# Performance work log

Hardware: AMD Instinct MI355X
Metric: run time of the kernel (lower is better)

The kernel has to match this reference:

```python
import jax, jax.numpy as jnp
import numpy as np

T, P, E, H = 200000, 100000, 600000, 256

def setup_inputs() -> dict:
    key = jax.random.key(0)
    ks = jax.random.split(key, 8)
    x = jax.random.normal(ks[0], (T, H), dtype=jnp.float32)
    points = jax.random.normal(ks[1], (P, 3), dtype=jnp.float32)
    triangles = jax.random.randint(ks[2], (T, 3), 0, P)
    triangle_edges = jax.random.randint(ks[3], (2, E), 0, T)
    din = H + 9
    W1 = jax.random.normal(ks[4], (din, H), dtype=jnp.float32) / np.sqrt(din)
    b1 = jnp.zeros((H,), dtype=jnp.float32)
    W2 = jax.random.normal(ks[5], (H, H), dtype=jnp.float32) / np.sqrt(H)
    b2 = jnp.zeros((H,), dtype=jnp.float32)
    return {"x": x, "points": points, "triangles": triangles,
            "triangle_edges": triangle_edges, "W1": W1, "b1": b1, "W2": W2, "b2": b2}

def reference(x, points, triangles, triangle_edges, W1, b1, W2, b2):
    # Per-triangle geometry: [T, 3(corners), 3(xyz)]
    tp = points[triangles]
    e_ij = tp[:, 0] - tp[:, 1]
    e_ik = tp[:, 0] - tp[:, 2]
    e_jk = tp[:, 1] - tp[:, 2]
    edge_vectors = jnp.stack([e_ij, e_ik, e_jk], axis=1)  # [T,3,3]
    t_max = jnp.max(edge_vectors, axis=1).astype(x.dtype)  # [T,3]
    t_min = jnp.min(edge_vectors, axis=1).astype(x.dtype)  # [T,3]
    barycenters = jnp.mean(tp, axis=1).astype(x.dtype)     # [T,3]

    src = triangle_edges[0]
    tgt = triangle_edges[1]
    # Relative geometric descriptor per edge: [E, 9]
    r_n_k = jnp.concatenate([t_min[src] - t_min[tgt],
                             t_max[src] - t_max[tgt],
                             barycenters[src] - barycenters[tgt]], axis=1)
    feature_diff = x[src] - x[tgt]                          # [E, H]
    mlp_in = jnp.concatenate([r_n_k, feature_diff], axis=1)  # [E, H+9]
    h = jax.nn.relu(mlp_in @ W1 + b1)
    mlp_out = h @ W2 + b2                                   # [E, H]
    # Scatter-add back to source triangles (order-independent sum)
    new_features = jax.ops.segment_sum(mlp_out, src, num_segments=x.shape[0])
    return new_features.astype(x.dtype)
```

## Files before the change

### kernel.cpp

```cpp
#include <hip/hip_runtime.h>
#include <stdint.h>

typedef float f32x4v __attribute__((ext_vector_type(4)));
typedef short short8v __attribute__((ext_vector_type(8)));

__device__ __forceinline__ float bf2f(unsigned short u) {
  union { uint32_t i; float f; } v; v.i = ((uint32_t)u) << 16; return v.f;
}
__device__ __forceinline__ unsigned short f2bf(float f) {
  union { float f; uint32_t i; } v; v.f = f;
  uint32_t x = v.i;
  uint32_t r = (x + 0x7FFFu + ((x >> 16) & 1u)) >> 16;
  return (unsigned short)r;
}

__global__ void zero_kernel(int* __restrict__ p, int n4) {
  int i = blockIdx.x * blockDim.x + threadIdx.x;
  int stride = gridDim.x * blockDim.x;
  for (; i < n4; i += stride) ((int4*)p)[i] = make_int4(0, 0, 0, 0);
}

__global__ void setup_kernel(const float* __restrict__ W1, const float* __restrict__ W2,
                             const float* __restrict__ points, const int* __restrict__ tri,
                             const int* __restrict__ te,
                             unsigned short* __restrict__ W1fT, unsigned short* __restrict__ W2T,
                             float* __restrict__ geo12, int* __restrict__ count,
                             int T, int E) {
  int i = blockIdx.x * blockDim.x + threadIdx.x;
  if (i < 256 * 288) {
    int n = i / 288, k = i % 288;
    float v = 0.f;
    if (k < 256) v = W1[(9 + k) * 256 + n];
    else if (k < 265) v = W1[(k - 256) * 256 + n];
    W1fT[i] = f2bf(v);
  }
  if (i < 256 * 256) {
    int n = i >> 8, k = i & 255;
    W2T[i] = f2bf(W2[k * 256 + n]);
  }
  if (i < T) {
    int t = i;
    int i0 = tri[3 * t], i1 = tri[3 * t + 1], i2 = tri[3 * t + 2];
    float g[12];
#pragma unroll
    for (int c = 0; c < 3; ++c) {
      float p0 = points[i0 * 3 + c], p1 = points[i1 * 3 + c], p2 = points[i2 * 3 + c];
      float e0 = p0 - p1, e1 = p0 - p2, e2 = p1 - p2;
      float mx = fmaxf(e0, fmaxf(e1, e2));
      float mn = fminf(e0, fminf(e1, e2));
      float bc = (p0 + p1 + p2) * (1.0f / 3.0f);
      g[c] = mn; g[3 + c] = mx; g[6 + c] = bc;
    }
    g[9] = 0.f; g[10] = 0.f; g[11] = 0.f;
    float4* o = (float4*)(geo12 + (size_t)t * 12);
    o[0] = make_float4(g[0], g[1], g[2], g[3]);
    o[1] = make_float4(g[4], g[5], g[6], g[7]);
    o[2] = make_float4(g[8], g[9], g[10], g[11]);
  }
  if (i < E) atomicAdd(&count[te[i]], 1);
}

__global__ void scan1_kernel(const int* __restrict__ count, int* __restrict__ incl,
                             int* __restrict__ blocksum, int T) {
  __shared__ int wsums[4];
  int tid = threadIdx.x, wave = tid >> 6, lane = tid & 63;
  int idx0 = blockIdx.x * 1024 + tid * 4;
  int c0 = 0, c1 = 0, c2 = 0, c3 = 0;
  if (idx0 + 3 < T) {
    int4 v = *(const int4*)(count + idx0);
    c0 = v.x; c1 = v.y; c2 = v.z; c3 = v.w;
  } else {
    if (idx0 < T) c0 = count[idx0];
    if (idx0 + 1 < T) c1 = count[idx0 + 1];
    if (idx0 + 2 < T) c2 = count[idx0 + 2];
  }
  int s = c0 + c1 + c2 + c3;
  int inclv = s;
#pragma unroll
  for (int off = 1; off < 64; off <<= 1) {
    int n = __shfl_up(inclv, off);
    if (lane >= off) inclv += n;
  }
  if (lane == 63) wsums[wave] = inclv;
  __syncthreads();
  int wbase = 0;
#pragma unroll
  for (int w = 0; w < 4; ++w) if (w < wave) wbase += wsums[w];
  int base = wbase + inclv - s;
  int e0 = base + c0, e1 = e0 + c1, e2 = e1 + c2, e3 = e2 + c3;
  if (idx0 < T) incl[idx0] = e0;
  if (idx0 + 1 < T) incl[idx0 + 1] = e1;
  if (idx0 + 2 < T) incl[idx0 + 2] = e2;
  if (idx0 + 3 < T) incl[idx0 + 3] = e3;
  if (tid == 255) blocksum[blockIdx.x] = wbase + inclv;
}

__global__ void scan2_kernel(const int* __restrict__ blocksum, int* __restrict__ blockbase, int nb) {
  __shared__ int wsums[4];
  int tid = threadIdx.x, wave = tid >> 6, lane = tid & 63;
  int v = (tid < nb) ? blocksum[tid] : 0;
  int inclv = v;
#pragma unroll
  for (int off = 1; off < 64; off <<= 1) {
    int n = __shfl_up(inclv, off);
    if (lane >= off) inclv += n;
  }
  if (lane == 63) wsums[wave] = inclv;
  __syncthreads();
  int wbase = 0;
#pragma unroll
  for (int w = 0; w < 4; ++w) if (w < wave) wbase += wsums[w];
  if (tid < nb) blockbase[tid] = wbase + inclv - v;
}

__global__ void scan3_kernel(const int* __restrict__ count, const int* __restrict__ incl,
                             const int* __restrict__ blockbase, int* __restrict__ offsets,
                             int* __restrict__ cursor, int T) {
  int idx = blockIdx.x * 1024 + threadIdx.x * 4;
  int bb = blockbase[blockIdx.x];
#pragma unroll
  for (int j = 0; j < 4; ++j) {
    int i = idx + j;
    if (i < T) {
      int o = incl[i] + bb;
      offsets[i + 1] = o;
      cursor[i] = o - count[i];
    }
  }
  if (blockIdx.x == 0 && threadIdx.x == 0) offsets[0] = 0;
}

__global__ void fill_kernel(const int* __restrict__ te, int* __restrict__ cursor,
                            int* __restrict__ tgt_list, int E) {
  int e = blockIdx.x * blockDim.x + threadIdx.x;
  if (e < E) {
    int s = te[e];
    int pos = atomicAdd(&cursor[s], 1);
    tgt_list[pos] = te[E + e];
  }
}

__launch_bounds__(512, 4)
__global__ void ugemm_kernel(const float* __restrict__ x, const float* __restrict__ geo12,
                             const unsigned short* __restrict__ W1fT,
                             unsigned short* __restrict__ U, int T) {
  __shared__ alignas(16) unsigned short Al[2][64][72];
  int m0 = blockIdx.x * 64;
  int tid = threadIdx.x;
  int wid = tid >> 6, lane = tid & 63;
  int srow = tid >> 3, cq = tid & 7;
  int l15 = lane & 15, lhi = lane >> 4;
  int nbase = wid * 32;
  f32x4v acc[4][2] = {};
  const unsigned short* bp[2];
#pragma unroll
  for (int nf = 0; nf < 2; ++nf)
    bp[nf] = W1fT + (size_t)(nbase + nf * 16 + l15) * 288 + 8 * lhi;
  int t = m0 + srow;
  const float* xrow = x + (size_t)t * 256 + cq * 8;

  auto loadx = [&](int kk, float* f) {
    const float* sp = xrow + kk * 64;
    float4 a = *(const float4*)sp;
    float4 b = *(const float4*)(sp + 4);
    f[0] = a.x; f[1] = a.y; f[2] = a.z; f[3] = a.w;
    f[4] = b.x; f[5] = b.y; f[6] = b.z; f[7] = b.w;
  };
  auto storeA = [&](int buf, float* f) {
    short8v v;
#pragma unroll
    for (int j = 0; j < 8; ++j) v[j] = (short)f2bf(f[j]);
    *(short8v*)(&Al[buf][srow][cq * 8]) = v;
  };

  {
    float f[8];
    loadx(0, f);
    storeA(0, f);
  }
  __syncthreads();

  for (int kk = 0; kk < 4; ++kk) {
    int cur = kk & 1;
    float fn[8];
    if (kk < 3) loadx(kk + 1, fn);
#pragma unroll
    for (int k2 = 0; k2 < 2; ++k2) {
      short8v a[4];
#pragma unroll
      for (int mi = 0; mi < 4; ++mi)
        a[mi] = *(const short8v*)(&Al[cur][mi * 16 + l15][k2 * 32 + 8 * lhi]);
#pragma unroll
      for (int nf = 0; nf < 2; ++nf) {
        short8v b = *(const short8v*)(bp[nf] + kk * 64 + k2 * 32);
#pragma unroll
        for (int mi = 0; mi < 4; ++mi)
          acc[mi][nf] = __builtin_amdgcn_mfma_f32_16x16x32_bf16(a[mi], b, acc[mi][nf], 0, 0, 0);
      }
    }
    if (kk < 3) storeA(cur ^ 1, fn);
    __syncthreads();
  }
  {
    float g[4];
    if (cq < 3) {
      float4 a = *(const float4*)(geo12 + (size_t)t * 12 + cq * 4);
      g[0] = a.x; g[1] = a.y; g[2] = a.z; g[3] = a.w;
    } else {
      g[0] = g[1] = g[2] = g[3] = 0.f;
    }
    ushort4 v;
    v.x = f2bf(g[0]); v.y = f2bf(g[1]); v.z = f2bf(g[2]); v.w = f2bf(g[3]);
    *(ushort4*)(&Al[0][srow][cq * 4]) = v;
    __syncthreads();
    short8v a[4];
#pragma unroll
    for (int mi = 0; mi < 4; ++mi)
      a[mi] = *(const short8v*)(&Al[0][mi * 16 + l15][8 * lhi]);
#pragma unroll
    for (int nf = 0; nf < 2; ++nf) {
      short8v b = *(const short8v*)(bp[nf] + 256);
#pragma unroll
      for (int mi = 0; mi < 4; ++mi)
        acc[mi][nf] = __builtin_amdgcn_mfma_f32_16x16x32_bf16(a[mi], b, acc[mi][nf], 0, 0, 0);
    }
  }
#pragma unroll
  for (int mi = 0; mi < 4; ++mi) {
#pragma unroll
    for (int i = 0; i < 4; ++i) {
      int m = m0 + mi * 16 + 4 * lhi + i;
#pragma unroll
      for (int nf = 0; nf < 2; ++nf) {
        int n = nbase + nf * 16 + l15;
        U[(size_t)m * 256 + n] = f2bf(acc[mi][nf][i]);
      }
    }
  }
}

__launch_bounds__(256, 4)
__global__ void gather_kernel(const unsigned short* __restrict__ U,
                              const int* __restrict__ offsets,
                              const int* __restrict__ tgt_list,
                              const float* __restrict__ b1,
                              unsigned short* __restrict__ sum_h, int T) {
  int gid = blockIdx.x * blockDim.x + threadIdx.x;
  int half = (T + 1) >> 1;
  int pair = gid >> 5;
  if (pair >= half) return;
  int c8 = (gid & 31) * 8;
  int tA = pair, tB = pair + half;
  bool hasRowB = tB < T;
  int begA = offsets[tA], endA = offsets[tA + 1];
  int begB = hasRowB ? offsets[tB] : 0, endB = hasRowB ? offsets[tB + 1] : 0;
  float b1r[8];
  {
    float4 a = *(const float4*)(b1 + c8);
    float4 b = *(const float4*)(b1 + c8 + 4);
    b1r[0] = a.x; b1r[1] = a.y; b1r[2] = a.z; b1r[3] = a.w;
    b1r[4] = b.x; b1r[5] = b.y; b1r[6] = b.z; b1r[7] = b.w;
  }
  short8v uva = *(const short8v*)(U + (size_t)tA * 256 + c8);
  short8v uvb = *(const short8v*)(U + (size_t)(hasRowB ? tB : tA) * 256 + c8);
  float uA[8], sA[8], uB[8], sB[8];
#pragma unroll
  for (int j = 0; j < 8; ++j) {
    uA[j] = bf2f((unsigned short)uva[j]) + b1r[j]; sA[j] = 0.f;
    uB[j] = bf2f((unsigned short)uvb[j]) + b1r[j]; sB[j] = 0.f;
  }
  int eiA = begA, eiB = begB;
  while (eiA < endA || eiB < endB) {
    bool hasA = eiA < endA, hasB = eiB < endB;
    int laA = hasA ? endA - 1 : 0;
    int laB = hasB ? endB - 1 : 0;
    int a0 = hasA ? eiA : 0;
    int a1 = hasA ? min(eiA + 1, laA) : 0;
    int a2 = hasA ? min(eiA + 2, laA) : 0;
    int a3 = hasA ? min(eiA + 3, laA) : 0;
    int b0 = hasB ? eiB : 0;
    int b1i = hasB ? min(eiB + 1, laB) : 0;
    int b2i = hasB ? min(eiB + 2, laB) : 0;
    int b3 = hasB ? min(eiB + 3, laB) : 0;
    int gA0 = tgt_list[a0], gA1 = tgt_list[a1], gA2 = tgt_list[a2], gA3 = tgt_list[a3];
    int gB0 = tgt_list[b0], gB1 = tgt_list[b1i], gB2 = tgt_list[b2i], gB3 = tgt_list[b3];
    short8v vA0 = *(const short8v*)(U + (size_t)gA0 * 256 + c8);
    short8v vA1 = *(const short8v*)(U + (size_t)gA1 * 256 + c8);
    short8v vA2 = *(const short8v*)(U + (size_t)gA2 * 256 + c8);
    short8v vA3 = *(const short8v*)(U + (size_t)gA3 * 256 + c8);
    short8v vB0 = *(const short8v*)(U + (size_t)gB0 * 256 + c8);
    short8v vB1 = *(const short8v*)(U + (size_t)gB1 * 256 + c8);
    short8v vB2 = *(const short8v*)(U + (size_t)gB2 * 256 + c8);
    short8v vB3 = *(const short8v*)(U + (size_t)gB3 * 256 + c8);
    float mA0 = hasA ? 1.f : 0.f;
    float mA1 = (hasA && eiA + 1 <= laA) ? 1.f : 0.f;
    float mA2 = (hasA && eiA + 2 <= laA) ? 1.f : 0.f;
    float mA3 = (hasA && eiA + 3 <= laA) ? 1.f : 0.f;
    float mB0 = hasB ? 1.f : 0.f;
    float mB1 = (hasB && eiB + 1 <= laB) ? 1.f : 0.f;
    float mB2 = (hasB && eiB + 2 <= laB) ? 1.f : 0.f;
    float mB3 = (hasB && eiB + 3 <= laB) ? 1.f : 0.f;
#pragma unroll
    for (int j = 0; j < 8; ++j) {
      sA[j] += mA0 * fmaxf(uA[j] - bf2f((unsigned short)vA0[j]), 0.f)
             + mA1 * fmaxf(uA[j] - bf2f((unsigned short)vA1[j]), 0.f)
             + mA2 * fmaxf(uA[j] - bf2f((unsigned short)vA2[j]), 0.f)
             + mA3 * fmaxf(uA[j] - bf2f((unsigned short)vA3[j]), 0.f);
      sB[j] += mB0 * fmaxf(uB[j] - bf2f((unsigned short)vB0[j]), 0.f)
             + mB1 * fmaxf(uB[j] - bf2f((unsigned short)vB1[j]), 0.f)
             + mB2 * fmaxf(uB[j] - bf2f((unsigned short)vB2[j]), 0.f)
             + mB3 * fmaxf(uB[j] - bf2f((unsigned short)vB3[j]), 0.f);
    }
    if (hasA) eiA += 4;
    if (hasB) eiB += 4;
  }
  short8v hva, hvb;
#pragma unroll
  for (int j = 0; j < 8; ++j) { hva[j] = (short)f2bf(sA[j]); hvb[j] = (short)f2bf(sB[j]); }
  *(short8v*)(sum_h + (size_t)tA * 256 + c8) = hva;
  if (hasRowB) *(short8v*)(sum_h + (size_t)tB * 256 + c8) = hvb;
}

__launch_bounds__(512, 4)
__global__ void out_gemm_kernel(const unsigned short* __restrict__ sum_h,
                                const unsigned short* __restrict__ W2T,
                                const int* __restrict__ count,
                                const float* __restrict__ b2,
                                float* __restrict__ out, int T) {
  __shared__ alignas(16) unsigned short Al[2][64][72];
  int m0 = blockIdx.x * 64;
  int tid = threadIdx.x;
  int wid = tid >> 6, lane = tid & 63;
  int srow = tid >> 3, cq = tid & 7;
  int l15 = lane & 15, lhi = lane >> 4;
  int nbase = wid * 32;
  f32x4v acc[4][2] = {};
  const unsigned short* bp[2];
  float b2r[2];
#pragma unroll
  for (int nf = 0; nf < 2; ++nf) {
    bp[nf] = W2T + (size_t)(nbase + nf * 16 + l15) * 256 + 8 * lhi;
    b2r[nf] = b2[nbase + nf * 16 + l15];
  }
  const unsigned short* arow = sum_h + (size_t)(m0 + srow) * 256 + cq * 8;
  *(short8v*)(&Al[0][srow][cq * 8]) = *(const short8v*)arow;
  __syncthreads();
  for (int kk = 0; kk < 4; ++kk) {
    int cur = kk & 1;
    short8v pre;
    if (kk < 3) pre = *(const short8v*)(arow + (kk + 1) * 64);
#pragma unroll
    for (int k2 = 0; k2 < 2; ++k2) {
      short8v a[4];
#pragma unroll
      for (int mi = 0; mi < 4; ++mi)
        a[mi] = *(const short8v*)(&Al[cur][mi * 16 + l15][k2 * 32 + 8 * lhi]);
#pragma unroll
      for (int nf = 0; nf < 2; ++nf) {
        short8v b = *(const short8v*)(bp[nf] + kk * 64 + k2 * 32);
#pragma unroll
        for (int mi = 0; mi < 4; ++mi)
          acc[mi][nf] = __builtin_amdgcn_mfma_f32_16x16x32_bf16(a[mi], b, acc[mi][nf], 0, 0, 0);
      }
    }
    if (kk < 3) *(short8v*)(&Al[cur ^ 1][srow][cq * 8]) = pre;
    __syncthreads();
  }
#pragma unroll
  for (int mi = 0; mi < 4; ++mi) {
#pragma unroll
    for (int i = 0; i < 4; ++i) {
      int t = m0 + mi * 16 + 4 * lhi + i;
      float cnt = (float)count[t];
#pragma unroll
      for (int nf = 0; nf < 2; ++nf) {
        int n = nbase + nf * 16 + l15;
        out[(size_t)t * 256 + n] = acc[mi][nf][i] + cnt * b2r[nf];
      }
    }
  }
}

extern "C" void kernel_launch(void* const* d_in, const int* in_sizes, int n_in,
                              void* d_out, int out_size, void* d_ws, size_t ws_size,
                              hipStream_t stream) {
  const float* x = (const float*)d_in[0];
  const float* points = (const float*)d_in[1];
  const int* triangles = (const int*)d_in[2];
  const int* te = (const int*)d_in[3];
  const float* W1 = (const float*)d_in[4];
  const float* b1 = (const float*)d_in[5];
  const float* W2 = (const float*)d_in[6];
  const float* b2 = (const float*)d_in[7];
  float* out = (float*)d_out;
  int T = in_sizes[0] / 256;
  int E = in_sizes[3] / 2;

  char* ws = (char*)d_ws;
  size_t off = 0;
  auto alloc = [&](size_t bytes) {
    void* p = ws + off;
    off = (off + bytes + 255) & ~(size_t)255;
    return p;
  };
  unsigned short* U     = (unsigned short*)alloc((size_t)T * 256 * 2);
  float*          geo12 = (float*)alloc(((size_t)T * 12 + 16) * 4);
  unsigned short* W1fT  = (unsigned short*)alloc((size_t)256 * 288 * 2);
  unsigned short* W2T   = (unsigned short*)alloc((size_t)256 * 256 * 2);
  int* count   = (int*)alloc((size_t)(T + 4) * 4);
  int* offsets = (int*)alloc((size_t)(T + 1) * 4);
  int* cursor  = (int*)alloc((size_t)T * 4);
  int* tgtl    = (int*)alloc((size_t)E * 4);
  int* incl    = (int*)alloc((size_t)T * 4);
  int* bsum    = (int*)alloc(256 * 4);
  int* bbase   = (int*)alloc(256 * 4);
  unsigned short* sum_h = (unsigned short*)alloc((size_t)T * 256 * 2);
  if (off > ws_size) return;

  int nb1 = (T + 1023) / 1024;
  hipMemsetAsync(nullptr, 0, 0, stream);
  zero_kernel<<<200, 256, 0, stream>>>(count, (T + 3) / 4);
  {
    int mx = max(E, max(T, 256 * 288));
    setup_kernel<<<(mx + 255) / 256, 256, 0, stream>>>(W1, W2, points, triangles, te,
                                                       W1fT, W2T, geo12, count, T, E);
  }
  scan1_kernel<<<nb1, 256, 0, stream>>>(count, incl, bsum, T);
  scan2_kernel<<<1, 256, 0, stream>>>(bsum, bbase, nb1);
  scan3_kernel<<<nb1, 256, 0, stream>>>(count, incl, bbase, offsets, cursor, T);
  fill_kernel<<<(E + 255) / 256, 256, 0, stream>>>(te, cursor, tgtl, E);
  ugemm_kernel<<<(T + 63) / 64, 512, 0, stream>>>(x, geo12, W1fT, U, T);
  {
    int half = (T + 1) >> 1;
    gather_kernel<<<(half * 32 + 255) / 256, 256, 0, stream>>>(U, offsets, tgtl, b1, sum_h, T);
  }
  out_gemm_kernel<<<(T + 63) / 64, 512, 0, stream>>>(sum_h, W2T, count, b2, out, T);
}
```

Baseline: 344.5 us.

## Stage out-GEMM A tiles with direct global-to-LDS loads and deepen ugemm prefetch

The output GEMM now fills its LDS A tile with `global_load_lds` DMA instead of loading into registers and then storing. It drops the row padding and uses an XOR swizzle on the 16-byte chunks so the MFMA fragment reads avoid bank conflicts. The U GEMM now prefetches x two K-chunks ahead in registers with a fully unrolled K loop, which raises register pressure. A no-op `hipMemsetAsync` is removed, and an unused `domfma` lambda is added as dead code.

```diff
diff --git a/kernel.cpp b/kernel.cpp
--- a/kernel.cpp
+++ b/kernel.cpp
@@ -172,18 +172,37 @@
     for (int j = 0; j < 8; ++j) v[j] = (short)f2bf(f[j]);
     *(short8v*)(&Al[buf][srow][cq * 8]) = v;
   };
-
+  auto domfma = [&](int buf) {
+#pragma unroll
+    for (int k2 = 0; k2 < 2; ++k2) {
+      short8v a[4];
+#pragma unroll
+      for (int mi = 0; mi < 4; ++mi)
+        a[mi] = *(const short8v*)(&Al[buf][mi * 16 + l15][k2 * 32 + 8 * lhi]);
+#pragma unroll
+      for (int nf = 0; nf < 2; ++nf) {
+        short8v b = *(const short8v*)(bp[nf] +  k2 * 32);
+#pragma unroll
+        for (int mi = 0; mi < 4; ++mi)
+          acc[mi][nf] = __builtin_amdgcn_mfma_f32_16x16x32_bf16(a[mi], b, acc[mi][nf], 0, 0, 0);
+      }
+    }
+  };
+  (void)domfma;
+
+  float fA[8], fB[8];
   {
-    float f[8];
-    loadx(0, f);
-    storeA(0, f);
-  }
+    float f0[8];
+    loadx(0, f0);
+    storeA(0, f0);
+  }
+  loadx(1, fA);
+  loadx(2, fB);
   __syncthreads();
 
+#pragma unroll
   for (int kk = 0; kk < 4; ++kk) {
     int cur = kk & 1;
-    float fn[8];
-    if (kk < 3) loadx(kk + 1, fn);
 #pragma unroll
     for (int k2 = 0; k2 < 2; ++k2) {
       short8v a[4];
@@ -198,7 +217,9 @@
           acc[mi][nf] = __builtin_amdgcn_mfma_f32_16x16x32_bf16(a[mi], b, acc[mi][nf], 0, 0, 0);
       }
     }
-    if (kk < 3) storeA(cur ^ 1, fn);
+    if (kk == 0) { storeA(1, fA); loadx(3, fA); }
+    else if (kk == 1) { storeA(0, fB); }
+    else if (kk == 2) { storeA(1, fA); }
     __syncthreads();
   }
   {
@@ -327,11 +348,11 @@
                                 const int* __restrict__ count,
                                 const float* __restrict__ b2,
                                 float* __restrict__ out, int T) {
-  __shared__ alignas(16) unsigned short Al[2][64][72];
+  __shared__ alignas(16) unsigned short Al[2][64][64];
   int m0 = blockIdx.x * 64;
   int tid = threadIdx.x;
   int wid = tid >> 6, lane = tid & 63;
-  int srow = tid >> 3, cq = tid & 7;
+  int srow = tid >> 3, slot = tid & 7;
   int l15 = lane & 15, lhi = lane >> 4;
   int nbase = wid * 32;
   f32x4v acc[4][2] = {};
@@ -342,19 +363,27 @@
     bp[nf] = W2T + (size_t)(nbase + nf * 16 + l15) * 256 + 8 * lhi;
     b2r[nf] = b2[nbase + nf * 16 + l15];
   }
-  const unsigned short* arow = sum_h + (size_t)(m0 + srow) * 256 + cq * 8;
-  *(short8v*)(&Al[0][srow][cq * 8]) = *(const short8v*)arow;
+  const unsigned short* gsrc = sum_h + (size_t)(m0 + srow) * 256 + (slot ^ (srow & 7)) * 8;
+  auto stage = [&](int buf, int kk) {
+    __builtin_amdgcn_global_load_lds(
+        (const __attribute__((address_space(1))) void*)(gsrc + kk * 64),
+        (__attribute__((address_space(3))) void*)((char*)&Al[buf][0][0] + wid * 1024),
+        16, 0, 0);
+  };
+  stage(0, 0);
   __syncthreads();
+#pragma unroll
   for (int kk = 0; kk < 4; ++kk) {
     int cur = kk & 1;
-    short8v pre;
-    if (kk < 3) pre = *(const short8v*)(arow + (kk + 1) * 64);
+    if (kk < 3) stage(cur ^ 1, kk + 1);
 #pragma unroll
     for (int k2 = 0; k2 < 2; ++k2) {
       short8v a[4];
 #pragma unroll
-      for (int mi = 0; mi < 4; ++mi)
-        a[mi] = *(const short8v*)(&Al[cur][mi * 16 + l15][k2 * 32 + 8 * lhi]);
+      for (int mi = 0; mi < 4; ++mi) {
+        int p = (k2 * 4 + lhi) ^ (l15 & 7);
+        a[mi] = *(const short8v*)(&Al[cur][mi * 16 + l15][p * 8]);
+      }
 #pragma unroll
       for (int nf = 0; nf < 2; ++nf) {
         short8v b = *(const short8v*)(bp[nf] + kk * 64 + k2 * 32);
@@ -363,7 +392,6 @@
           acc[mi][nf] = __builtin_amdgcn_mfma_f32_16x16x32_bf16(a[mi], b, acc[mi][nf], 0, 0, 0);
       }
     }
-    if (kk < 3) *(short8v*)(&Al[cur ^ 1][srow][cq * 8]) = pre;
     __syncthreads();
   }
 #pragma unroll
@@ -418,7 +446,6 @@
   if (off > ws_size) return;
 
   int nb1 = (T + 1023) / 1024;
-  hipMemsetAsync(nullptr, 0, 0, stream);
   zero_kernel<<<200, 256, 0, stream>>>(count, (T + 3) / 4);
   {
     int mx = max(E, max(T, 256 * 288));
```

After: 345.2 us. No clear change (+0.2%).
